# Kernel optimization log

Hardware: AMD Instinct MI355X
Metric: run time of the kernel (lower is better)

The kernel has to match this reference:

```python
import jax, jax.numpy as jnp
import numpy as np

# wav2vec-large feature extractor conv spec: (kernel, stride), 512 channels each
LAYERS = [(10, 5), (8, 4), (4, 2), (4, 2), (4, 2)]
C = 512
BLUR = 0.05   # geomloss SamplesLoss default
N_ITER = 50   # fixed sinkhorn iterations (reference for eps-scaling loop)


def conv1d(x, w, stride):
    # x: [B, Cin, T], w: [Cout, Cin, K]
    return jax.lax.conv_general_dilated(
        x, w, window_strides=(stride,), padding='VALID',
        dimension_numbers=('NCH', 'OIH', 'NCH'))


def group_norm1(x, gamma, beta, eps=1e-5):
    # GroupNorm with 1 group over [C, T] per sample, per-channel affine
    mu = x.mean(axis=(1, 2), keepdims=True)
    var = x.var(axis=(1, 2), keepdims=True)
    return (x - mu) * jax.lax.rsqrt(var + eps) * gamma[None, :, None] + beta[None, :, None]


def features(wav, Ws, gs, bs):
    h = wav[:, None, :]  # [B,1,T]
    for (k, s), W, g, b in zip(LAYERS, Ws, gs, bs):
        h = jax.nn.relu(group_norm1(conv1d(h, W, s), g, b))
    return h  # [B, 512, T']


def sq_cost(a, b):
    # 0.5 * ||a_i - b_j||^2  (geomloss p=2 cost); a:[B,N,D], b:[B,M,D]
    aa = (a * a).sum(-1)
    bb = (b * b).sum(-1)
    ab = jnp.einsum('bnd,bmd->bnm', a, b)
    return 0.5 * jnp.maximum(aa[:, :, None] + bb[:, None, :] - 2.0 * ab, 0.0)


def ot_eps(Cm, eps):
    # entropic OT with uniform weights, log-domain sinkhorn; Cm: [B,N,M]
    B, N, M = Cm.shape
    loga = jnp.full((B, N), -jnp.log(N), dtype=Cm.dtype)
    logb = jnp.full((B, M), -jnp.log(M), dtype=Cm.dtype)
    f0 = jnp.zeros((B, N), Cm.dtype)
    g0 = jnp.zeros((B, M), Cm.dtype)

    def body(carry, _):
        f, g = carry
        g = -eps * jax.nn.logsumexp(loga[:, :, None] + (f[:, :, None] - Cm) / eps, axis=1)
        f = -eps * jax.nn.logsumexp(logb[:, None, :] + (g[:, None, :] - Cm) / eps, axis=2)
        return (f, g), None

    (f, g), _ = jax.lax.scan(body, (f0, g0), None, length=N_ITER)
    a = jnp.exp(loga)
    b = jnp.exp(logb)
    return (a * f).sum(-1) + (b * g).sum(-1)  # [B]


def sinkhorn_divergence(x, y):
    eps = BLUR ** 2
    return (ot_eps(sq_cost(x, y), eps)
            - 0.5 * ot_eps(sq_cost(x, x), eps)
            - 0.5 * ot_eps(sq_cost(y, y), eps))


def setup_inputs() -> dict:
    key = jax.random.key(0)
    ks = jax.random.split(key, 20)
    B, T = 16, 32000
    inp = {
        'y_hat': jax.random.normal(ks[0], (B, T), jnp.float32),
        'y': jax.random.normal(ks[1], (B, T), jnp.float32),
    }
    cin = 1
    for i, (k, s) in enumerate(LAYERS):
        inp[f'W{i}'] = jax.random.normal(ks[2 + i], (C, cin, k), jnp.float32) * 0.05
        inp[f'g{i}'] = jnp.ones((C,), jnp.float32)
        inp[f'b{i}'] = jnp.zeros((C,), jnp.float32)
        cin = C
    return inp


def reference(y_hat, y, W0, W1, W2, W3, W4, g0, g1, g2, g3, g4, b0, b1, b2, b3, b4):
    Ws = [W0, W1, W2, W3, W4]
    gs = [g0, g1, g2, g3, g4]
    bs = [b0, b1, b2, b3, b4]
    fx = features(y_hat, Ws, gs, bs)  # [B,512,T'] -> point cloud N=512, D=T'
    fy = features(y, Ws, gs, bs)
    return sinkhorn_divergence(fx, fy)  # [B]
```

## Files before the change

### kernel.cpp

```cpp
#include <hip/hip_runtime.h>

typedef unsigned int uint;
typedef unsigned short ushort;
using half8v  = __attribute__((ext_vector_type(8))) _Float16;
using half4v  = __attribute__((ext_vector_type(4))) _Float16;
using float4v = __attribute__((ext_vector_type(4))) float;

#define EPS_SINK 0.0025f
#define INV_EPS_SINK 400.0f
#define EPS_LOG512 0.015595811562598769f

static const size_t O_W1   = 0ull;
static const size_t O_W2   = 4194304ull;
static const size_t O_W3   = 6291456ull;
static const size_t O_W4   = 8388608ull;
static const size_t O_H0   = 20971520ull;
static const size_t O_H1   = 125829120ull;
static const size_t O_H2   = 20971520ull;
static const size_t O_H3   = 34045952ull;
static const size_t O_FEATX= 152010752ull;
static const size_t O_FEATY= 158498816ull;
static const size_t O_STATS= 164986880ull;
static const size_t O_CXY  = 0ull;
static const size_t O_CTXY = 8388608ull;
static const size_t O_CXX  = 16777216ull;
static const size_t O_CYY  = 25165824ull;
static const size_t O_AAX  = 33554432ull;
static const size_t O_AAY  = 33587200ull;
static const size_t O_F    = 33619968ull;
static const size_t O_G    = 33718272ull;

#define GLOAD_LDS16(gp, lp) __builtin_amdgcn_global_load_lds( \
    (const __attribute__((address_space(1))) void*)(gp),       \
    (__attribute__((address_space(3))) void*)(lp), 16, 0, 0)

__global__ __launch_bounds__(256) void prep_w(
    const float* __restrict__ W1, const float* __restrict__ W2,
    const float* __restrict__ W3, const float* __restrict__ W4,
    _Float16* __restrict__ w1, _Float16* __restrict__ w2,
    _Float16* __restrict__ w3, _Float16* __restrict__ w4)
{
    const int layer = blockIdx.y;
    const int e = blockIdx.x * 256 + threadIdx.x;
    float v[8];
    _Float16* dh;
    if (layer == 0) {
        const float4 a = *(const float4*)(W1 + (size_t)e * 8);
        const float4 c = *(const float4*)(W1 + (size_t)e * 8 + 4);
        v[0]=a.x; v[1]=a.y; v[2]=a.z; v[3]=a.w; v[4]=c.x; v[5]=c.y; v[6]=c.z; v[7]=c.w;
        dh = w1;
    } else {
        if (e >= 131072) return;
        const float* W = (layer == 1) ? W2 : (layer == 2) ? W3 : W4;
        dh = (layer == 1) ? w2 : (layer == 2) ? w3 : w4;
        const int oc = e >> 8, icp = e & 255;
        const float4 a = *(const float4*)(W + ((size_t)oc * 512 + icp * 2) * 4);
        const float4 c = *(const float4*)(W + ((size_t)oc * 512 + icp * 2 + 1) * 4);
        v[0]=a.x; v[1]=c.x; v[2]=a.y; v[3]=c.y; v[4]=a.z; v[5]=c.z; v[6]=a.w; v[7]=c.w;
    }
    half8v hi;
#pragma unroll
    for (int k = 0; k < 8; ++k) hi[k] = (_Float16)v[k];
    *(half8v*)(dh + (size_t)e * 8) = hi;
}

__global__ __launch_bounds__(256) void conv0_store(
    const float* __restrict__ wav, const float* __restrict__ W0,
    _Float16* __restrict__ h0, float* __restrict__ stats)
{
    __shared__ float LW[5120];
    __shared__ float red[2][256];
    const int tid = threadIdx.x;
    for (int e = tid; e < 5120; e += 256) LW[e] = W0[e];

    const int b = blockIdx.y;
    const int t = blockIdx.x * 256 + tid;
    const bool valid = (t < 6399);
    float xv[10];
#pragma unroll
    for (int d = 0; d < 10; ++d) xv[d] = 0.f;
    if (valid) {
        const float* wp = wav + (size_t)b * 32000 + (size_t)t * 5;
#pragma unroll
        for (int d = 0; d < 10; ++d) xv[d] = wp[d];
    }
    __syncthreads();

    float lsum = 0.f, lsq = 0.f;
    _Float16* hb = h0 + (size_t)b * 512 * 6400;
    for (int oc = 0; oc < 512; ++oc) {
        float a = 0.f;
#pragma unroll
        for (int d = 0; d < 10; ++d) a += LW[oc * 10 + d] * xv[d];
        if (valid) {
            hb[(size_t)oc * 6400 + t] = (_Float16)a;
            lsum += a; lsq += a * a;
        }
    }
    red[0][tid] = lsum; red[1][tid] = lsq;
    __syncthreads();
    for (int s2 = 128; s2 > 0; s2 >>= 1) {
        if (tid < s2) { red[0][tid] += red[0][tid + s2]; red[1][tid] += red[1][tid + s2]; }
        __syncthreads();
    }
    if (tid == 0) {
        atomicAdd(&stats[2 * b], red[0][0]);
        atomicAdd(&stats[2 * b + 1], red[1][0]);
    }
}

__global__ __launch_bounds__(256, 4) void conv1_mfma(
    const _Float16* __restrict__ h0,
    const _Float16* __restrict__ w1,
    const float* __restrict__ stats0,
    const float* __restrict__ gamma0, const float* __restrict__ beta0,
    _Float16* __restrict__ oh, float* __restrict__ stats1)
{
    __shared__ _Float16 LW[2][2][4][128][8];
    __shared__ float LSC[512], LSH[512];
    __shared__ float red[2][256];

    const int tid  = threadIdx.x;
    const int lane = tid & 63, wv = tid >> 6;
    const int m    = lane & 15, quad = lane >> 4;
    const int wv2  = wv >> 1, wvt = wv & 1;

    const int raw = blockIdx.x;
    const int cid = (raw & 7) * 104 + (raw >> 3);
    const int b   = cid / 52;
    const int r2  = cid - b * 52;
    const int xt  = r2 >> 2, yt = r2 & 3;
    const int ocb = yt * 128;
    const int t0  = xt * 128;
    const int Lout = 1598;

    {
        const float invN = 1.f / (512.f * 6399.f);
        const float mu = stats0[2 * b] * invN;
        const float var = stats0[2 * b + 1] * invN - mu * mu;
        const float rs = rsqrtf(var + 1e-5f);
        for (int ic = tid; ic < 512; ic += 256) {
            const float sc = rs * gamma0[ic];
            LSC[ic] = sc;
            LSH[ic] = beta0[ic] - mu * sc;
        }
    }

    float4v acc[4][4];
#pragma unroll
    for (int i = 0; i < 4; ++i)
#pragma unroll
        for (int j = 0; j < 4; ++j) acc[i][j] = (float4v){0.f, 0.f, 0.f, 0.f};

    const _Float16* hb = h0 + (size_t)b * 512 * 6400;
    const int gbase = t0 * 4;
    const _Float16* px = hb + (size_t)quad * 6400 + gbase + (wvt * 64 + m) * 4;

    const _Float16* wsrc[4];
#pragma unroll
    for (int r = 0; r < 4; ++r) {
        const int e = wv * 4 + r;
        const int oh2 = e & 1, q = (e >> 1) & 3, k32l = e >> 3;
        wsrc[r] = w1 + ((size_t)(ocb + oh2 * 64 + lane) * 512 + (k32l * 4 + q)) * 8;
    }
    auto stageW = [&](int buf) {
#pragma unroll
        for (int r = 0; r < 4; ++r) {
            const int e = wv * 4 + r;
            const int oh2 = e & 1, q = (e >> 1) & 3, k32l = e >> 3;
            GLOAD_LDS16(wsrc[r], &LW[buf][k32l][q][oh2 * 64][0]);
            wsrc[r] += 64;
        }
    };

    stageW(0);
    __syncthreads();

    for (int it = 0; it < 64; ++it) {
        const int buf = it & 1;
        if (it < 63) stageW(buf ^ 1);
#pragma unroll
        for (int k32l = 0; k32l < 2; ++k32l) {
            half8v a4[4], bfv[4];
#pragma unroll
            for (int i = 0; i < 4; ++i)
                a4[i] = *(const half8v*)&LW[buf][k32l][quad][wv2 * 64 + i * 16 + m][0];
            const int ic = quad + 4 * k32l + 8 * it;
            const _Float16 sch = (_Float16)LSC[ic];
            const _Float16 shh = (_Float16)LSH[ic];
            const _Float16* pr = px + (size_t)k32l * 25600;
#pragma unroll
            for (int j = 0; j < 4; ++j) {
                half8v xv = *(const half8v*)(pr + j * 64);
#pragma unroll
                for (int k = 0; k < 8; ++k) {
                    const _Float16 v = xv[k] * sch + shh;
                    xv[k] = (v > (_Float16)0.f) ? v : (_Float16)0.f;
                }
                bfv[j] = xv;
            }
#pragma unroll
            for (int i = 0; i < 4; ++i)
#pragma unroll
                for (int j = 0; j < 4; ++j)
                    acc[i][j] = __builtin_amdgcn_mfma_f32_16x16x32_f16(a4[i], bfv[j], acc[i][j], 0, 0, 0);
        }
        px += 51200;
        __syncthreads();
    }

    float lsum = 0.f, lsq = 0.f;
    uint* ohU = (uint*)oh;
#pragma unroll
    for (int i = 0; i < 4; ++i) {
        const int ocb2 = ocb + wv2 * 64 + i * 16 + quad * 4;
#pragma unroll
        for (int j = 0; j < 4; ++j) {
            const int t = t0 + wvt * 64 + j * 16 + m;
            if (t < Lout) {
#pragma unroll
                for (int pr = 0; pr < 2; ++pr) {
                    const float v0 = acc[i][j][pr * 2], v1 = acc[i][j][pr * 2 + 1];
                    union { uint u; _Float16 h[2]; } pk;
                    pk.h[0] = (_Float16)v0; pk.h[1] = (_Float16)v1;
                    const uint p = (uint)((ocb2 >> 1) + pr);
                    ohU[((size_t)(b * 256 + p)) * Lout + t] = pk.u;
                    lsum += v0 + v1; lsq += v0 * v0 + v1 * v1;
                }
            }
        }
    }
    red[0][tid] = lsum; red[1][tid] = lsq;
    __syncthreads();
    for (int s2 = 128; s2 > 0; s2 >>= 1) {
        if (tid < s2) { red[0][tid] += red[0][tid + s2]; red[1][tid] += red[1][tid + s2]; }
        __syncthreads();
    }
    if (tid == 0) {
        atomicAdd(&stats1[2 * b], red[0][0]);
        atomicAdd(&stats1[2 * b + 1], red[1][0]);
    }
}

template <bool PAIRED>
__global__ __launch_bounds__(256, 4) void conv_mfma(
    const _Float16* __restrict__ x,
    const _Float16* __restrict__ w,
    const float* __restrict__ statsP,
    const float* __restrict__ gammaP, const float* __restrict__ betaP,
    _Float16* __restrict__ oh, _Float16* __restrict__ ofeat,
    float* __restrict__ statsO, int Lin, int Lout, int nx)
{
    __shared__ _Float16 LW[2][2][4][128][8];
    __shared__ float LN[256][4];
    __shared__ float red[2][256];

    const int tid  = threadIdx.x;
    const int lane = tid & 63, wv = tid >> 6;
    const int m    = lane & 15, quad = lane >> 4;
    const int wv2  = wv >> 1, wvt = wv & 1;

    const int raw = blockIdx.x;
    const int chunk = (nx * 64) >> 3;
    const int cid = (raw & 7) * chunk + (raw >> 3);
    const int perb = nx * 4;
    const int b   = cid / perb;
    const int r2  = cid - b * perb;
    const int xt  = r2 >> 2, yt = r2 & 3;
    const int ocb = yt * 128;
    const int t0  = xt * 64;

    {
        const float invN = 1.f / (512.f * (float)Lin);
        const float mu = statsP[2 * b] * invN;
        const float var = statsP[2 * b + 1] * invN - mu * mu;
        const float rs = rsqrtf(var + 1e-5f);
        const int c0 = 2 * tid, c1 = 2 * tid + 1;
        const float sc0 = rs * gammaP[c0], sc1 = rs * gammaP[c1];
        LN[tid][0] = sc0; LN[tid][1] = betaP[c0] - mu * sc0;
        LN[tid][2] = sc1; LN[tid][3] = betaP[c1] - mu * sc1;
    }

    float4v acc[4][2];
#pragma unroll
    for (int i = 0; i < 4; ++i)
#pragma unroll
        for (int j = 0; j < 2; ++j) acc[i][j] = (float4v){0.f, 0.f, 0.f, 0.f};

    const size_t rstride = (size_t)Lin * 2;
    const _Float16* px = x + ((size_t)(b * 256) + quad) * rstride
                           + t0 * 4 + (wvt * 32 + m) * 4;

    const _Float16* wsrc[4];
#pragma unroll
    for (int r = 0; r < 4; ++r) {
        const int e = wv * 4 + r;
        const int oh2 = e & 1, q = (e >> 1) & 3, k32l = e >> 3;
        wsrc[r] = w + ((size_t)(ocb + oh2 * 64 + lane) * 256 + (k32l * 4 + q)) * 8;
    }
    auto stageW = [&](int buf) {
#pragma unroll
        for (int r = 0; r < 4; ++r) {
            const int e = wv * 4 + r;
            const int oh2 = e & 1, q = (e >> 1) & 3, k32l = e >> 3;
            GLOAD_LDS16(wsrc[r], &LW[buf][k32l][q][oh2 * 64][0]);
            wsrc[r] += 64;
        }
    };
    auto loadX = [&](half8v (&xr)[4], const _Float16* p) {
#pragma unroll
        for (int k32l = 0; k32l < 2; ++k32l)
#pragma unroll
            for (int j = 0; j < 2; ++j)
                xr[k32l * 2 + j] = *(const half8v*)(p + (size_t)k32l * 4 * rstride + j * 64);
    };
    auto compute = [&](int buf, half8v (&xr)[4], int plB) {
#pragma unroll
        for (int k32l = 0; k32l < 2; ++k32l) {
            half8v a4[4];
#pragma unroll
            for (int i = 0; i < 4; ++i)
                a4[i] = *(const half8v*)&LW[buf][k32l][quad][wv2 * 64 + i * 16 + m][0];
            const int pl = plB + quad + 4 * k32l;
            const _Float16 s0 = (_Float16)LN[pl][0], h0v = (_Float16)LN[pl][1];
            const _Float16 s1 = (_Float16)LN[pl][2], h1v = (_Float16)LN[pl][3];
            half8v xn[2];
#pragma unroll
            for (int j = 0; j < 2; ++j) {
                half8v xv = xr[k32l * 2 + j];
#pragma unroll
                for (int k = 0; k < 8; ++k) {
                    const _Float16 v = xv[k] * ((k & 1) ? s1 : s0) + ((k & 1) ? h1v : h0v);
                    xv[k] = (v > (_Float16)0.f) ? v : (_Float16)0.f;
                }
                xn[j] = xv;
            }
#pragma unroll
            for (int i = 0; i < 4; ++i)
#pragma unroll
                for (int j = 0; j < 2; ++j)
                    acc[i][j] = __builtin_amdgcn_mfma_f32_16x16x32_f16(a4[i], xn[j], acc[i][j], 0, 0, 0);
        }
    };

    half8v xrA[4], xrB[4];
    loadX(xrA, px); px += 8 * rstride;
    stageW(0);
    __syncthreads();

    for (int it = 0; it < 32; it += 2) {
        stageW(1);
        loadX(xrB, px); px += 8 * rstride;
        compute(0, xrA, 8 * it);
        __syncthreads();
        if (it + 2 < 32) {
            stageW(0);
            loadX(xrA, px);
        }
        px += 8 * rstride;
        compute(1, xrB, 8 * (it + 1));
        __syncthreads();
    }

    float lsum = 0.f, lsq = 0.f;
    uint* ohU = (uint*)oh;
#pragma unroll
    for (int i = 0; i < 4; ++i) {
        const int ocb2 = ocb + wv2 * 64 + i * 16 + quad * 4;
#pragma unroll
        for (int j = 0; j < 2; ++j) {
            const int t = t0 + wvt * 32 + j * 16 + m;
            if (t < Lout) {
                if (PAIRED) {
#pragma unroll
                    for (int pr = 0; pr < 2; ++pr) {
                        const float v0 = acc[i][j][pr * 2], v1 = acc[i][j][pr * 2 + 1];
                        union { uint u; _Float16 h[2]; } pk;
                        pk.h[0] = (_Float16)v0; pk.h[1] = (_Float16)v1;
                        const uint p = (uint)((ocb2 >> 1) + pr);
                        ohU[((size_t)(b * 256 + p)) * Lout + t] = pk.u;
                        lsum += v0 + v1; lsq += v0 * v0 + v1 * v1;
                    }
                } else {
#pragma unroll
                    for (int r = 0; r < 4; ++r) {
                        const float v = acc[i][j][r];
                        ofeat[((size_t)(b * 512 + ocb2 + r)) * 224 + t] = (_Float16)v;
                        lsum += v; lsq += v * v;
                    }
                }
            }
        }
    }
    red[0][tid] = lsum; red[1][tid] = lsq;
    __syncthreads();
    for (int s2 = 128; s2 > 0; s2 >>= 1) {
        if (tid < s2) { red[0][tid] += red[0][tid + s2]; red[1][tid] += red[1][tid + s2]; }
        __syncthreads();
    }
    if (tid == 0) {
        atomicAdd(&statsO[2 * b], red[0][0]);
        atomicAdd(&statsO[2 * b + 1], red[1][0]);
    }
}

__global__ __launch_bounds__(256) void norm_feat(
    _Float16* __restrict__ h, const float* __restrict__ stats,
    const float* __restrict__ gamma, const float* __restrict__ beta)
{
    const int row = blockIdx.y;
    const int b = row >> 9, oc = row & 511;
    const int t = threadIdx.x;
    if (t >= 198) return;
    const float invN = 1.f / (512.f * 198.f);
    const float mu = stats[2 * b] * invN;
    const float var = stats[2 * b + 1] * invN - mu * mu;
    const float rs = rsqrtf(var + 1e-5f);
    const float sc = rs * gamma[oc];
    const float sh = beta[oc] - mu * sc;
    const size_t i = (size_t)row * 224 + t;
    const float v = (float)h[i] * sc + sh;
    h[i] = (_Float16)(v > 0.f ? v : 0.f);
}

__global__ __launch_bounds__(256) void aa_kernel(
    const _Float16* __restrict__ fX, const _Float16* __restrict__ fY,
    float* __restrict__ aaX, float* __restrict__ aaY)
{
    const int wave = threadIdx.x >> 6, lane = threadIdx.x & 63;
    const int R = blockIdx.x * 4 + wave;
    const _Float16* f = (R < 8192) ? fX : fY;
    const int r = R & 8191;
    const _Float16* row = f + (size_t)r * 224;
    float s = 0.f;
    if (lane < 56) {
        const half4v v = *(const half4v*)(row + lane * 4);
#pragma unroll
        for (int k = 0; k < 4; ++k) { const float x = (float)v[k]; s += x * x; }
    }
#pragma unroll
    for (int off = 32; off > 0; off >>= 1) s += __shfl_xor(s, off);
    if (lane == 0) ((R < 8192) ? aaX : aaY)[r] = s;
}

__global__ __launch_bounds__(256) void cost_kernel(
    const _Float16* __restrict__ fX, const _Float16* __restrict__ fY,
    const float* __restrict__ aaX, const float* __restrict__ aaY,
    _Float16* __restrict__ Cxy, _Float16* __restrict__ Cxx,
    _Float16* __restrict__ Cyy, _Float16* __restrict__ CTxy)
{
    const int z = blockIdx.y;
    const int mat = z >> 4, b = z & 15;
    const int nt = blockIdx.x & 3, mt = blockIdx.x >> 2;
    if (mat != 0 && nt > mt) return;
    const _Float16 *P, *Q; const float *aP, *aQ;
    _Float16 *Cm, *CT;
    if (mat == 0)      { P = fX; Q = fY; aP = aaX; aQ = aaY; Cm = Cxy; CT = CTxy; }
    else if (mat == 1) { P = fX; Q = fX; aP = aaX; aQ = aaX; Cm = Cxx; CT = (nt < mt) ? Cxx : nullptr; }
    else               { P = fY; Q = fY; aP = aaY; aQ = aaY; Cm = Cyy; CT = (nt < mt) ? Cyy : nullptr; }

    const int tid = threadIdx.x, lane = tid & 63, wv = tid >> 6;
    const int m16 = lane & 15, quad = lane >> 4;
    const int wv2 = wv >> 1, wvt = wv & 1;
    const int nb = nt * 128 + wv2 * 64;
    const int mb = mt * 128 + wvt * 64;
    const _Float16* Pb = P + (size_t)b * 512 * 224;
    const _Float16* Qb = Q + (size_t)b * 512 * 224;

    float4v acc[4][4];
#pragma unroll
    for (int i = 0; i < 4; ++i)
#pragma unroll
        for (int j = 0; j < 4; ++j) acc[i][j] = (float4v){0.f, 0.f, 0.f, 0.f};

    for (int k32 = 0; k32 < 7; ++k32) {
        const int ko = k32 * 32 + quad * 8;
        half8v a4[4], b4[4];
#pragma unroll
        for (int i = 0; i < 4; ++i)
            a4[i] = *(const half8v*)(Pb + (size_t)(nb + i * 16 + m16) * 224 + ko);
#pragma unroll
        for (int j = 0; j < 4; ++j)
            b4[j] = *(const half8v*)(Qb + (size_t)(mb + j * 16 + m16) * 224 + ko);
#pragma unroll
        for (int i = 0; i < 4; ++i)
#pragma unroll
            for (int j = 0; j < 4; ++j)
                acc[i][j] = __builtin_amdgcn_mfma_f32_16x16x32_f16(a4[i], b4[j], acc[i][j], 0, 0, 0);
    }

#pragma unroll
    for (int i = 0; i < 4; ++i) {
        const int nrow0 = nb + i * 16 + quad * 4;
        float aa4[4];
#pragma unroll
        for (int r = 0; r < 4; ++r) aa4[r] = aP[b * 512 + nrow0 + r];
#pragma unroll
        for (int j = 0; j < 4; ++j) {
            const int mcol = mb + j * 16 + m16;
            const float bbm = aQ[b * 512 + mcol];
#pragma unroll
            for (int r = 0; r < 4; ++r) {
                const int n = nrow0 + r;
                float c = 50.f * fmaxf(aa4[r] + bbm - 2.f * acc[i][j][r], 0.f);
                c = fminf(c, 65000.f);
                const _Float16 ch = (_Float16)c;
                Cm[((size_t)(b * 512 + n)) * 512 + mcol] = ch;
                if (CT) CT[((size_t)(b * 512 + mcol)) * 512 + n] = ch;
            }
        }
    }
}

static __device__ __forceinline__ void sink_rows(
    float* __restrict__ dst, const float* __restrict__ src,
    const _Float16* __restrict__ Mb, int p, int i0, int lane)
{
    const float* sp = src + (size_t)p * 512;
    float s8[8];
    {
        const float4 sa = *(const float4*)&sp[lane * 8];
        const float4 sb = *(const float4*)&sp[lane * 8 + 4];
        s8[0]=sa.x*400.f; s8[1]=sa.y*400.f; s8[2]=sa.z*400.f; s8[3]=sa.w*400.f;
        s8[4]=sb.x*400.f; s8[5]=sb.y*400.f; s8[6]=sb.z*400.f; s8[7]=sb.w*400.f;
    }
#pragma unroll
    for (int rr = 0; rr < 4; ++rr) {
        const int i = i0 + rr;
        const half8v rv = *(const half8v*)(Mb + (size_t)i * 512 + lane * 8);
        float a8[8];
#pragma unroll
        for (int k = 0; k < 8; ++k) a8[k] = fmaf(-4.f, (float)rv[k], s8[k]);
        float mx = a8[0];
#pragma unroll
        for (int k = 1; k < 8; ++k) mx = fmaxf(mx, a8[k]);
#pragma unroll
        for (int off = 32; off > 0; off >>= 1) mx = fmaxf(mx, __shfl_xor(mx, off));
        float ss = 0.f;
#pragma unroll
        for (int k = 0; k < 8; ++k) ss += __expf(a8[k] - mx);
#pragma unroll
        for (int off = 32; off > 0; off >>= 1) ss += __shfl_xor(ss, off);
        if (lane == 0)
            dst[(size_t)p * 512 + i] = EPS_LOG512 - EPS_SINK * (mx + logf(ss));
    }
}

__global__ __launch_bounds__(256) void sink_update(
    float* __restrict__ dst, const float* __restrict__ src,
    const _Float16* __restrict__ M0, const _Float16* __restrict__ M1,
    const _Float16* __restrict__ M2)
{
    const int p = blockIdx.y;
    const int mat = p >> 4, b = p & 15;
    const _Float16* M = ((mat == 0) ? M0 : ((mat == 1) ? M1 : M2)) + (size_t)b * 512 * 512;
    const int wave = threadIdx.x >> 6, lane = threadIdx.x & 63;
    const int i0 = blockIdx.x * 16 + wave * 4;
    sink_rows(dst, src, M, p, i0, lane);
}

__global__ __launch_bounds__(256) void final_kernel(
    const float* __restrict__ f, const float* __restrict__ g,
    float* __restrict__ out)
{
    const int b = blockIdx.x, tid = threadIdx.x;
    __shared__ float red[256];
    float a = 0.f;
    for (int n = tid; n < 512; n += 256) {
        const float xy = f[(0 * 16 + b) * 512 + n] + g[(0 * 16 + b) * 512 + n];
        const float xx = f[(1 * 16 + b) * 512 + n] + g[(1 * 16 + b) * 512 + n];
        const float yy = f[(2 * 16 + b) * 512 + n] + g[(2 * 16 + b) * 512 + n];
        a += xy - 0.5f * (xx + yy);
    }
    red[tid] = a;
    __syncthreads();
    for (int s2 = 128; s2 > 0; s2 >>= 1) {
        if (tid < s2) red[tid] += red[tid + s2];
        __syncthreads();
    }
    if (tid == 0) out[b] = red[0] * (1.0f / 512.0f);
}

extern "C" void kernel_launch(void* const* d_in, const int* in_sizes, int n_in,
                              void* d_out, int out_size, void* d_ws, size_t ws_size,
                              hipStream_t stream)
{
    (void)in_sizes; (void)n_in; (void)out_size; (void)ws_size;
    char* ws = (char*)d_ws;
    const float* yhat = (const float*)d_in[0];
    const float* ysig = (const float*)d_in[1];
    const float* Wl[5]; const float* gl[5]; const float* bl[5];
    for (int i = 0; i < 5; ++i) {
        Wl[i] = (const float*)d_in[2 + 3 * i];
        gl[i] = (const float*)d_in[3 + 3 * i];
        bl[i] = (const float*)d_in[4 + 3 * i];
    }
    float* out = (float*)d_out;
    float* statsA = (float*)(ws + O_STATS);

    _Float16* w1 = (_Float16*)(ws + O_W1);
    _Float16* w2 = (_Float16*)(ws + O_W2);
    _Float16* w3 = (_Float16*)(ws + O_W3);
    _Float16* w4 = (_Float16*)(ws + O_W4);
    _Float16* h0 = (_Float16*)(ws + O_H0);
    _Float16* h1 = (_Float16*)(ws + O_H1);
    _Float16* h2 = (_Float16*)(ws + O_H2);
    _Float16* h3 = (_Float16*)(ws + O_H3);

    hipMemsetAsync(statsA, 0, 512 * sizeof(float), stream);
    hipMemsetAsync(ws + O_FEATX, 0, 16 * 512 * 224 * 2, stream);
    hipMemsetAsync(ws + O_FEATY, 0, 16 * 512 * 224 * 2, stream);
    prep_w<<<dim3(1024, 4), 256, 0, stream>>>(Wl[1], Wl[2], Wl[3], Wl[4],
        w1, w2, w3, w4);

    for (int s = 0; s < 2; ++s) {
        const float* wav = (s == 0) ? yhat : ysig;
        float* st = statsA + (size_t)s * 160;
        _Float16* ft = (_Float16*)(ws + ((s == 0) ? O_FEATX : O_FEATY));

        conv0_store<<<dim3(25, 16), 256, 0, stream>>>(wav, Wl[0], h0, st);

        conv1_mfma<<<dim3(832), 256, 0, stream>>>(
            h0, w1, st, gl[0], bl[0], h1, st + 32);

        conv_mfma<true><<<dim3(832), 256, 0, stream>>>(
            h1, w2, st + 32, gl[1], bl[1], h2, nullptr, st + 64, 1598, 798, 13);

        conv_mfma<true><<<dim3(448), 256, 0, stream>>>(
            h2, w3, st + 64, gl[2], bl[2], h3, nullptr, st + 96, 798, 398, 7);

        conv_mfma<false><<<dim3(256), 256, 0, stream>>>(
            h3, w4, st + 96, gl[3], bl[3], nullptr, ft, st + 128, 398, 198, 4);

        norm_feat<<<dim3(1, 8192), 256, 0, stream>>>(
            ft, st + 128, gl[4], bl[4]);
    }

    _Float16* featX = (_Float16*)(ws + O_FEATX);
    _Float16* featY = (_Float16*)(ws + O_FEATY);
    aa_kernel<<<4096, 256, 0, stream>>>(featX, featY, (float*)(ws + O_AAX), (float*)(ws + O_AAY));
    cost_kernel<<<dim3(16, 48), 256, 0, stream>>>(
        featX, featY, (float*)(ws + O_AAX), (float*)(ws + O_AAY),
        (_Float16*)(ws + O_CXY), (_Float16*)(ws + O_CXX), (_Float16*)(ws + O_CYY),
        (_Float16*)(ws + O_CTXY));

    hipMemsetAsync(ws + O_F, 0, 2 * 24576 * sizeof(float), stream);

    float* fptr = (float*)(ws + O_F);
    float* gptr = (float*)(ws + O_G);
    _Float16* cxy  = (_Float16*)(ws + O_CXY);
    _Float16* ctxy = (_Float16*)(ws + O_CTXY);
    _Float16* cxx  = (_Float16*)(ws + O_CXX);
    _Float16* cyy  = (_Float16*)(ws + O_CYY);

    for (int it = 0; it < 50; ++it) {
        sink_update<<<dim3(32, 48), 256, 0, stream>>>(gptr, fptr, ctxy, cxx, cyy);
        sink_update<<<dim3(32, 48), 256, 0, stream>>>(fptr, gptr, cxy, cxx, cyy);
    }

    final_kernel<<<16, 256, 0, stream>>>(fptr, gptr, out);
}
```

Measured before the change: 1.691 ms.

## Widen conv_mfma time tile, vectorize GN-ReLU, use exp2/log2 in sinkhorn

Doubles the time tile of conv_mfma from 64 to 128 outputs per block (4x4 accumulators), halving grid sizes for layers 2-4. It also drops the register double-buffered X prefetch in favour of direct loads inside the loop. The GroupNorm+ReLU prologue is vectorized with half8 FMA and an elementwise max. The sinkhorn row logsumexp is rewritten in base 2 with pre-scaled constants so it can use exp2/log2 directly. The trade-offs are fewer blocks, which lowers occupancy and parallelism on smaller layers, more accumulator registers, and less latency hiding for the X loads.

```diff
diff --git a/kernel.cpp b/kernel.cpp
--- a/kernel.cpp
+++ b/kernel.cpp
@@ -7,8 +7,10 @@
 using float4v = __attribute__((ext_vector_type(4))) float;
 
 #define EPS_SINK 0.0025f
-#define INV_EPS_SINK 400.0f
 #define EPS_LOG512 0.015595811562598769f
+#define S_SCALE_L2   577.0780163555852f
+#define C_SCALE_L2  (-5.770780163555852f)
+#define EPS_LN2      0.0017328679513999f
 
 static const size_t O_W1   = 0ull;
 static const size_t O_W2   = 4194304ull;
@@ -34,6 +36,14 @@
     (const __attribute__((address_space(1))) void*)(gp),       \
     (__attribute__((address_space(3))) void*)(lp), 16, 0, 0)
 
+static __device__ __forceinline__ half8v gn_relu8(half8v xv, half8v sc8, half8v sh8)
+{
+    half8v v = xv * sc8 + sh8;
+    const half8v z = (half8v){(_Float16)0.f, (_Float16)0.f, (_Float16)0.f, (_Float16)0.f,
+                              (_Float16)0.f, (_Float16)0.f, (_Float16)0.f, (_Float16)0.f};
+    return __builtin_elementwise_max(v, z);
+}
+
 __global__ __launch_bounds__(256) void prep_w(
     const float* __restrict__ W1, const float* __restrict__ W2,
     const float* __restrict__ W3, const float* __restrict__ W4,
@@ -186,19 +196,14 @@
             for (int i = 0; i < 4; ++i)
                 a4[i] = *(const half8v*)&LW[buf][k32l][quad][wv2 * 64 + i * 16 + m][0];
             const int ic = quad + 4 * k32l + 8 * it;
-            const _Float16 sch = (_Float16)LSC[ic];
-            const _Float16 shh = (_Float16)LSH[ic];
+            const _Float16 s = (_Float16)LSC[ic];
+            const _Float16 h = (_Float16)LSH[ic];
+            const half8v sc8 = (half8v){s, s, s, s, s, s, s, s};
+            const half8v sh8 = (half8v){h, h, h, h, h, h, h, h};
             const _Float16* pr = px + (size_t)k32l * 25600;
 #pragma unroll
-            for (int j = 0; j < 4; ++j) {
-                half8v xv = *(const half8v*)(pr + j * 64);
-#pragma unroll
-                for (int k = 0; k < 8; ++k) {
-                    const _Float16 v = xv[k] * sch + shh;
-                    xv[k] = (v > (_Float16)0.f) ? v : (_Float16)0.f;
-                }
-                bfv[j] = xv;
-            }
+            for (int j = 0; j < 4; ++j)
+                bfv[j] = gn_relu8(*(const half8v*)(pr + j * 64), sc8, sh8);
 #pragma unroll
             for (int i = 0; i < 4; ++i)
 #pragma unroll
@@ -268,7 +273,7 @@
     const int r2  = cid - b * perb;
     const int xt  = r2 >> 2, yt = r2 & 3;
     const int ocb = yt * 128;
-    const int t0  = xt * 64;
+    const int t0  = xt * 128;
 
     {
         const float invN = 1.f / (512.f * (float)Lin);
@@ -281,15 +286,15 @@
         LN[tid][2] = sc1; LN[tid][3] = betaP[c1] - mu * sc1;
     }
 
-    float4v acc[4][2];
+    float4v acc[4][4];
 #pragma unroll
     for (int i = 0; i < 4; ++i)
 #pragma unroll
-        for (int j = 0; j < 2; ++j) acc[i][j] = (float4v){0.f, 0.f, 0.f, 0.f};
+        for (int j = 0; j < 4; ++j) acc[i][j] = (float4v){0.f, 0.f, 0.f, 0.f};
 
     const size_t rstride = (size_t)Lin * 2;
     const _Float16* px = x + ((size_t)(b * 256) + quad) * rstride
-                           + t0 * 4 + (wvt * 32 + m) * 4;
+                           + t0 * 4 + (wvt * 64 + m) * 4;
 
     const _Float16* wsrc[4];
 #pragma unroll
@@ -307,58 +312,35 @@
             wsrc[r] += 64;
         }
     };
-    auto loadX = [&](half8v (&xr)[4], const _Float16* p) {
-#pragma unroll
-        for (int k32l = 0; k32l < 2; ++k32l)
-#pragma unroll
-            for (int j = 0; j < 2; ++j)
-                xr[k32l * 2 + j] = *(const half8v*)(p + (size_t)k32l * 4 * rstride + j * 64);
-    };
-    auto compute = [&](int buf, half8v (&xr)[4], int plB) {
+
+    stageW(0);
+    __syncthreads();
+
+    for (int it = 0; it < 32; ++it) {
+        const int buf = it & 1;
+        if (it < 31) stageW(buf ^ 1);
 #pragma unroll
         for (int k32l = 0; k32l < 2; ++k32l) {
-            half8v a4[4];
+            half8v a4[4], bfv[4];
 #pragma unroll
             for (int i = 0; i < 4; ++i)
                 a4[i] = *(const half8v*)&LW[buf][k32l][quad][wv2 * 64 + i * 16 + m][0];
-            const int pl = plB + quad + 4 * k32l;
+            const int pl = quad + 4 * k32l + 8 * it;
             const _Float16 s0 = (_Float16)LN[pl][0], h0v = (_Float16)LN[pl][1];
             const _Float16 s1 = (_Float16)LN[pl][2], h1v = (_Float16)LN[pl][3];
-            half8v xn[2];
-#pragma unroll
-            for (int j = 0; j < 2; ++j) {
-                half8v xv = xr[k32l * 2 + j];
-#pragma unroll
-                for (int k = 0; k < 8; ++k) {
-                    const _Float16 v = xv[k] * ((k & 1) ? s1 : s0) + ((k & 1) ? h1v : h0v);
-                    xv[k] = (v > (_Float16)0.f) ? v : (_Float16)0.f;
-                }
-                xn[j] = xv;
-            }
+            const half8v sc8 = (half8v){s0, s1, s0, s1, s0, s1, s0, s1};
+            const half8v sh8 = (half8v){h0v, h1v, h0v, h1v, h0v, h1v, h0v, h1v};
+            const _Float16* pr = px + (size_t)k32l * 4 * rstride;
+#pragma unroll
+            for (int j = 0; j < 4; ++j)
+                bfv[j] = gn_relu8(*(const half8v*)(pr + j * 64), sc8, sh8);
 #pragma unroll
             for (int i = 0; i < 4; ++i)
 #pragma unroll
-                for (int j = 0; j < 2; ++j)
-                    acc[i][j] = __builtin_amdgcn_mfma_f32_16x16x32_f16(a4[i], xn[j], acc[i][j], 0, 0, 0);
-        }
-    };
-
-    half8v xrA[4], xrB[4];
-    loadX(xrA, px); px += 8 * rstride;
-    stageW(0);
-    __syncthreads();
-
-    for (int it = 0; it < 32; it += 2) {
-        stageW(1);
-        loadX(xrB, px); px += 8 * rstride;
-        compute(0, xrA, 8 * it);
-        __syncthreads();
-        if (it + 2 < 32) {
-            stageW(0);
-            loadX(xrA, px);
+                for (int j = 0; j < 4; ++j)
+                    acc[i][j] = __builtin_amdgcn_mfma_f32_16x16x32_f16(a4[i], bfv[j], acc[i][j], 0, 0, 0);
         }
         px += 8 * rstride;
-        compute(1, xrB, 8 * (it + 1));
         __syncthreads();
     }
 
@@ -368,8 +350,8 @@
     for (int i = 0; i < 4; ++i) {
         const int ocb2 = ocb + wv2 * 64 + i * 16 + quad * 4;
 #pragma unroll
-        for (int j = 0; j < 2; ++j) {
-            const int t = t0 + wvt * 32 + j * 16 + m;
+        for (int j = 0; j < 4; ++j) {
+            const int t = t0 + wvt * 64 + j * 16 + m;
             if (t < Lout) {
                 if (PAIRED) {
 #pragma unroll
@@ -521,8 +503,8 @@
     {
         const float4 sa = *(const float4*)&sp[lane * 8];
         const float4 sb = *(const float4*)&sp[lane * 8 + 4];
-        s8[0]=sa.x*400.f; s8[1]=sa.y*400.f; s8[2]=sa.z*400.f; s8[3]=sa.w*400.f;
-        s8[4]=sb.x*400.f; s8[5]=sb.y*400.f; s8[6]=sb.z*400.f; s8[7]=sb.w*400.f;
+        s8[0]=sa.x*S_SCALE_L2; s8[1]=sa.y*S_SCALE_L2; s8[2]=sa.z*S_SCALE_L2; s8[3]=sa.w*S_SCALE_L2;
+        s8[4]=sb.x*S_SCALE_L2; s8[5]=sb.y*S_SCALE_L2; s8[6]=sb.z*S_SCALE_L2; s8[7]=sb.w*S_SCALE_L2;
     }
 #pragma unroll
     for (int rr = 0; rr < 4; ++rr) {
@@ -530,7 +512,7 @@
         const half8v rv = *(const half8v*)(Mb + (size_t)i * 512 + lane * 8);
         float a8[8];
 #pragma unroll
-        for (int k = 0; k < 8; ++k) a8[k] = fmaf(-4.f, (float)rv[k], s8[k]);
+        for (int k = 0; k < 8; ++k) a8[k] = fmaf(C_SCALE_L2, (float)rv[k], s8[k]);
         float mx = a8[0];
 #pragma unroll
         for (int k = 1; k < 8; ++k) mx = fmaxf(mx, a8[k]);
@@ -538,11 +520,11 @@
         for (int off = 32; off > 0; off >>= 1) mx = fmaxf(mx, __shfl_xor(mx, off));
         float ss = 0.f;
 #pragma unroll
-        for (int k = 0; k < 8; ++k) ss += __expf(a8[k] - mx);
+        for (int k = 0; k < 8; ++k) ss += exp2f(a8[k] - mx);
 #pragma unroll
         for (int off = 32; off > 0; off >>= 1) ss += __shfl_xor(ss, off);
         if (lane == 0)
-            dst[(size_t)p * 512 + i] = EPS_LOG512 - EPS_SINK * (mx + logf(ss));
+            dst[(size_t)p * 512 + i] = EPS_LOG512 - EPS_LN2 * (mx + log2f(ss));
     }
 }
 
@@ -623,14 +605,14 @@
         conv1_mfma<<<dim3(832), 256, 0, stream>>>(
             h0, w1, st, gl[0], bl[0], h1, st + 32);
 
-        conv_mfma<true><<<dim3(832), 256, 0, stream>>>(
-            h1, w2, st + 32, gl[1], bl[1], h2, nullptr, st + 64, 1598, 798, 13);
-
         conv_mfma<true><<<dim3(448), 256, 0, stream>>>(
-            h2, w3, st + 64, gl[2], bl[2], h3, nullptr, st + 96, 798, 398, 7);
-
-        conv_mfma<false><<<dim3(256), 256, 0, stream>>>(
-            h3, w4, st + 96, gl[3], bl[3], nullptr, ft, st + 128, 398, 198, 4);
+            h1, w2, st + 32, gl[1], bl[1], h2, nullptr, st + 64, 1598, 798, 7);
+
+        conv_mfma<true><<<dim3(256), 256, 0, stream>>>(
+            h2, w3, st + 64, gl[2], bl[2], h3, nullptr, st + 96, 798, 398, 4);
+
+        conv_mfma<false><<<dim3(128), 256, 0, stream>>>(
+            h3, w4, st + 96, gl[3], bl[3], nullptr, ft, st + 128, 398, 198, 2);
 
         norm_feat<<<dim3(1, 8192), 256, 0, stream>>>(
             ft, st + 128, gl[4], bl[4]);
```

After: 1.795 ms. 6.1% more time.
